# Kernel tuning notes

Hardware: AMD Instinct MI355X
Metric: run time of the kernel (lower is better)

Reference implementation:

```python
import jax, jax.numpy as jnp
import numpy as np

B, S = 64, 512
VOCAB, D, H, NH = 50000, 256, 256, 4
MAX_DUR = 12.0
SCALE_RATE = 1.0


def setup_inputs() -> dict:
    key = jax.random.key(0)
    ks = jax.random.split(key, 12)
    s = 1.0 / np.sqrt(H)
    inp = {
        "src": jax.random.randint(ks[0], (B, S), 0, VOCAB),
        "input_len": jax.random.randint(ks[1], (B,), 1, S + 1),
        "fix_src": jax.random.uniform(ks[2], (B, S), jnp.float32) * MAX_DUR,
        "emb_table": jax.random.normal(ks[3], (VOCAB, D), jnp.float32) * 0.02,
        "Wi": jax.random.uniform(ks[4], (H, D), jnp.float32, -s, s),
        "bi": jax.random.uniform(ks[5], (H,), jnp.float32, -s, s),
        "Wh": jax.random.uniform(ks[6], (H, NH * H), jnp.float32, -s, s),
        "bh": jax.random.uniform(ks[7], (H,), jnp.float32, -s, s),
        "fc1_W": jax.random.uniform(ks[8], (D, NH * H), jnp.float32, -s, s),
        "fc1_b": jax.random.uniform(ks[9], (D,), jnp.float32, -s, s),
        "fc2_W": jax.random.uniform(ks[10], (2, D), jnp.float32, -s, s),
        "fc2_b": jax.random.uniform(ks[11], (2,), jnp.float32, -s, s),
    }
    return inp


def _forward(src, input_len, fix_src, emb_table, Wi, bi, Wh, bh, fc1_W, fc1_b, fc2_W, fc2_b):
    emb = emb_table[src]                      # [B, S, D]
    offsets = jnp.arange(NH, dtype=emb.dtype) * (MAX_DUR / NH)  # [NH]
    h0 = jnp.zeros((NH, B, H), emb.dtype)

    def step(h, xd):
        x, d = xd                             # x [B,D], d [B]
        hcat = jnp.swapaxes(h, 0, 1).reshape(B, NH * H)
        cand = jnp.tanh(x @ Wi.T + bi + hcat @ Wh.T + bh)        # [B,H]
        g = jax.nn.sigmoid(d[:, None] * SCALE_RATE - offsets)    # [B,NH]
        gt = g.T[:, :, None]                                     # [NH,B,1]
        h_new = gt * cand[None, :, :] + (1.0 - gt) * h           # [NH,B,H]
        out = jnp.swapaxes(h_new, 0, 1).reshape(B, NH * H)
        return h_new, out

    xs = (jnp.swapaxes(emb, 0, 1), fix_src.T)  # [S,B,D], [S,B]
    _, outs = jax.lax.scan(step, h0, xs)       # [S, B, NH*H]
    outs = jnp.swapaxes(outs, 0, 1)            # [B, S, NH*H]
    sel = outs[jnp.arange(B), input_len - 1]   # gather at last valid step, [B, NH*H]
    hid = jnp.tanh(sel @ fc1_W.T + fc1_b)      # [B, D]
    return hid @ fc2_W.T + fc2_b               # [B, 2]


def reference(src, input_len, fix_src, emb_table, Wi, bi, Wh, bh, fc1_W, fc1_b, fc2_W, fc2_b):
    return _forward(src, input_len, fix_src, emb_table, Wi, bi, Wh, bh, fc1_W, fc1_b, fc2_W, fc2_b)
```

## Files before the change

kernel.cpp:

```cpp
#include <hip/hip_runtime.h>
#include <stdint.h>

constexpr int BB = 64;
constexpr int SS = 512;
constexpr int DD = 256;
constexpr int HH = 256;
constexpr int NHH = 4;
constexpr int KK = 1024;

constexpr int TT = 512;

typedef _Float16 f16;
typedef _Float16 f16x2 __attribute__((ext_vector_type(2)));
typedef _Float16 half8 __attribute__((ext_vector_type(8)));
typedef float f32x4 __attribute__((ext_vector_type(4)));

__device__ inline float dot2p(uint32_t a, uint32_t b, float c) {
  f16x2 av = __builtin_bit_cast(f16x2, a);
  f16x2 bv = __builtin_bit_cast(f16x2, b);
#if defined(__has_builtin)
#if __has_builtin(__builtin_amdgcn_fdot2)
  return __builtin_amdgcn_fdot2(av, bv, c, false);
#else
  return c + (float)av.x * (float)bv.x + (float)av.y * (float)bv.y;
#endif
#else
  return c + (float)av.x * (float)bv.x + (float)av.y * (float)bv.y;
#endif
}

__device__ inline float dot8(uint4 w, uint4 a, float c) {
  c = dot2p(w.x, a.x, c);
  c = dot2p(w.y, a.y, c);
  c = dot2p(w.z, a.z, c);
  c = dot2p(w.w, a.w, c);
  return c;
}

__device__ inline uint32_t pack2(float a, float b) {
  f16x2 v;
  v.x = (f16)a;
  v.y = (f16)b;
  return __builtin_bit_cast(uint32_t, v);
}

__device__ inline float fast_tanh(float x) {
  x = fminf(fmaxf(x, -15.f), 15.f);
  float e = __expf(2.f * x);
  return 1.f - 2.f / (e + 1.f);
}

__device__ __host__ inline int chunk_of(int p, int wv) {
  if (wv == 0) return 2 * p;
  if (wv == 7) return 2 * p + 1;
  return (2 * p + 1 + wv) & 7;
}

__global__ void k_pack_wq(const float* __restrict__ Wh, uint4* __restrict__ Wq) {
  int gid = blockIdx.x * blockDim.x + threadIdx.x;
  int p = gid >> 13;
  int m = (gid >> 9) & 15;
  int t = gid & 511;
  int j = m >> 2, u = m & 3;
  int wv = t >> 6, l = t & 63;
  int cw = chunk_of(p, wv);
  const float* s = Wh + (size_t)(64 * p + l) * KK + 256 * j + 32 * cw + 8 * u;
  uint4 w;
  w.x = pack2(s[0], s[1]);
  w.y = pack2(s[2], s[3]);
  w.z = pack2(s[4], s[5]);
  w.w = pack2(s[6], s[7]);
  Wq[gid] = w;
}

__global__ void k_transpose8(const float* __restrict__ src, float* __restrict__ dst,
                             int C, int total) {
  int gid = blockIdx.x * blockDim.x + threadIdx.x;
  if (gid >= total) return;
  int r = gid & 255, c = gid >> 8;
  dst[gid] = src[r * C + c];
}

__global__ void k_cvt_f16(const float* __restrict__ src, f16* __restrict__ dst,
                          int total) {
  int gid = blockIdx.x * blockDim.x + threadIdx.x;
  if (gid >= total) return;
  dst[gid] = (f16)src[gid];
}

__global__ __launch_bounds__(256) void k_u_mfma(
    const int* __restrict__ src, const float* __restrict__ emb,
    const f16* __restrict__ wif, const float* __restrict__ bi,
    const float* __restrict__ bh, const int* __restrict__ input_len,
    f16* __restrict__ U) {
  __shared__ __align__(16) char xls[32768];
  const int row0 = blockIdx.x * 64;
  const int b = row0 >> 9;
  if ((row0 & 511) >= input_len[b]) return;
  const int t = threadIdx.x;
  const int w = t >> 6, l = t & 63;

  for (int rr = 0; rr < 16; ++rr) {
    int r = w * 16 + rr;
    int srcid = src[row0 + r];
    const float4 x = *(const float4*)(emb + (size_t)srcid * DD + l * 4);
    uint2 dw;
    dw.x = pack2(x.x, x.y);
    dw.y = pack2(x.z, x.w);
    int byte = (r * 512 + l * 8) ^ ((r & 7) << 4);
    *(uint2*)(xls + byte) = dw;
  }
  __syncthreads();

  const int lm = l & 15, lk = l >> 4;
  const int arow = w * 16 + lm;
  const int xs = (arow & 7) << 4;

  for (int ct = 0; ct < 16; ++ct) {
    const int o = ct * 16 + lm;
    f32x4 acc = {0.f, 0.f, 0.f, 0.f};
    const f16* bp = wif + (size_t)o * 256 + lk * 8;
#pragma unroll
    for (int kt = 0; kt < 8; ++kt) {
      int ab = (arow * 512 + kt * 64 + lk * 16) ^ xs;
      half8 af = *(const half8*)(xls + ab);
      half8 bf = *(const half8*)(bp + kt * 32);
      acc = __builtin_amdgcn_mfma_f32_16x16x32_f16(af, bf, acc, 0, 0, 0);
    }
    float bias = bi[o] + bh[o];
#pragma unroll
    for (int reg = 0; reg < 4; ++reg) {
      int grow = row0 + w * 16 + lk * 4 + reg;
      U[(size_t)grow * HH + o] = (f16)(acc[reg] + bias);
    }
  }
}

__global__ void __attribute__((amdgpu_flat_work_group_size(512, 512),
                               amdgpu_waves_per_eu(2, 2)))
k_recurrence(
    const uint4* __restrict__ Wq, const f16* __restrict__ U,
    const float* __restrict__ fix_src, const int* __restrict__ input_len,
    const float* __restrict__ fc1T, const float* __restrict__ fc1_b,
    const float* __restrict__ fc2_W, const float* __restrict__ fc2_b,
    float* __restrict__ out, uint32_t* __restrict__ Cex,
    float* __restrict__ FPg, int* __restrict__ Flg) {
  __shared__ __align__(16) char arena[61440];
  f16* cbufX = (f16*)arena;
  uint4* cvecX = (uint4*)arena;
  float* part = (float*)(arena + 512);
  float* partials = (float*)(arena + 512);
  float* hbuf = (float*)(arena + 16896);
  float* fsbuf = (float*)(arena + 17920);

  const int idx = blockIdx.x;
  const int b = idx & 63;
  const int p = idx >> 6;
  const int t = threadIdx.x;
  const int wv = t >> 6, l = t & 63;
  const int out_i = t & 255, ch2 = t >> 8;

  const int cw = chunk_of(p, wv);
  const int q = cw >> 1, half = cw & 1;

  uint4 w[16];
  {
    const uint4* wp = Wq + (p * 16) * TT + t;
#pragma unroll
    for (int m = 0; m < 16; ++m) {
      const uint4* a = wp + m * TT;
      asm volatile("global_load_dwordx4 %0, %1, off"
                   : "=v"(w[m]) : "v"(a) : "memory");
    }
    asm volatile("s_waitcnt vmcnt(0)" ::: "memory");
  }

  float v0 = 0.f, v1 = 0.f, v2 = 0.f, v3 = 0.f;
  float h0 = 0.f, h1 = 0.f, h2 = 0.f, h3 = 0.f;
  float cprev = 0.f, unew = 0.f;

  const int len = input_len[b];
  const f16* Ub = U + (size_t)b * SS * HH;
  const float* fsb = fix_src + b * SS;

  fsbuf[t] = fsb[t];
  if (wv == 0) {
    float c0 = fast_tanh((float)Ub[64 * p + l]);
    f16 chv = (f16)c0;
    cprev = (float)chv;
    if (l < 32) cbufX[2 * p * 32 + l] = chv;
    uint32_t dwp =
        ((uint32_t)__builtin_bit_cast(unsigned short, chv) << 16) | 1u;
    __hip_atomic_store(&Cex[b * 256 + p * 64 + l], dwp, __ATOMIC_RELAXED,
                       __HIP_MEMORY_SCOPE_AGENT);
  }
  __syncthreads();

#pragma unroll 1
  for (int s = 0; s < len; ++s) {
#pragma unroll
    for (int m = 0; m < 16; ++m)
      asm volatile("" : "+v"(w[m].x), "+v"(w[m].y), "+v"(w[m].z), "+v"(w[m].w));

    const int par = s & 1;
    const uint32_t tag = (uint32_t)((s + 1) & 0xffff);
    float g0 = 0.f, g1 = 0.f, g2 = 0.f, g3 = 0.f;

    if (wv == 0) {
      const float dval = fsbuf[s];
      g0 = 1.f / (1.f + __expf(0.f - dval));
      g1 = 1.f / (1.f + __expf(3.f - dval));
      g2 = 1.f / (1.f + __expf(6.f - dval));
      g3 = 1.f / (1.f + __expf(9.f - dval));
      h0 = g0 * cprev + (1.f - g0) * h0;
      h1 = g1 * cprev + (1.f - g1) * h1;
      h2 = g2 * cprev + (1.f - g2) * h2;
      h3 = g3 * cprev + (1.f - g3) * h3;
      int sn = (s + 1 < len) ? (s + 1) : s;
      unew = (float)Ub[(size_t)sn * HH + 64 * p + l];
    } else {
      if (l < 32) {
        uint32_t* addr = &Cex[((par * 64 + b) * 4 + q) * 64 + 32 * half + l];
        uint32_t dw;
        do {
          dw = __hip_atomic_load(addr, __ATOMIC_RELAXED,
                                 __HIP_MEMORY_SCOPE_AGENT);
        } while ((dw & 0xffffu) != tag);
        cbufX[cw * 32 + l] = __builtin_bit_cast(f16, (unsigned short)(dw >> 16));
      }
    }

    {
      const uint4* ap = cvecX + cw * 4;
      uint4 a0 = ap[0], a1 = ap[1], a2 = ap[2], a3 = ap[3];
      float ac0 = 0.f, ac1 = 0.f, ac2 = 0.f, ac3 = 0.f;
      ac0 = dot8(w[0], a0, ac0);  ac0 = dot8(w[1], a1, ac0);
      ac0 = dot8(w[2], a2, ac0);  ac0 = dot8(w[3], a3, ac0);
      ac1 = dot8(w[4], a0, ac1);  ac1 = dot8(w[5], a1, ac1);
      ac1 = dot8(w[6], a2, ac1);  ac1 = dot8(w[7], a3, ac1);
      ac2 = dot8(w[8], a0, ac2);  ac2 = dot8(w[9], a1, ac2);
      ac2 = dot8(w[10], a2, ac2); ac2 = dot8(w[11], a3, ac2);
      ac3 = dot8(w[12], a0, ac3); ac3 = dot8(w[13], a1, ac3);
      ac3 = dot8(w[14], a2, ac3); ac3 = dot8(w[15], a3, ac3);
      float* pr = part + par * 2048 + cw * 256;
      pr[l] = ac0;
      pr[64 + l] = ac1;
      pr[128 + l] = ac2;
      pr[192 + l] = ac3;
    }
    __syncthreads();

    if (wv == 0) {
      float s0 = 0.f, s1 = 0.f, s2 = 0.f, s3 = 0.f;
      const float* pb = part + par * 2048;
#pragma unroll
      for (int kc = 0; kc < 8; ++kc) {
        const float* pr = pb + kc * 256;
        s0 += pr[l];
        s1 += pr[64 + l];
        s2 += pr[128 + l];
        s3 += pr[192 + l];
      }
      v0 = g0 * s0 + (1.f - g0) * v0;
      v1 = g1 * s1 + (1.f - g1) * v1;
      v2 = g2 * s2 + (1.f - g2) * v2;
      v3 = g3 * s3 + (1.f - g3) * v3;
      float c = fast_tanh(unew + (v0 + v1 + v2 + v3));
      f16 chv = (f16)c;
      cprev = (float)chv;
      uint32_t dwp =
          ((uint32_t)__builtin_bit_cast(unsigned short, chv) << 16) |
          (uint32_t)((s + 2) & 0xffff);
      __hip_atomic_store(&Cex[(((s + 1) & 1) * 64 + b) * 256 + p * 64 + l],
                         dwp, __ATOMIC_RELAXED, __HIP_MEMORY_SCOPE_AGENT);
      if (l < 32) cbufX[2 * p * 32 + l] = chv;
    }
  }

  if (wv == 0) {
    hbuf[l] = h0;
    hbuf[64 + l] = h1;
    hbuf[128 + l] = h2;
    hbuf[192 + l] = h3;
  }
  __syncthreads();
  {
    float acc = 0.f;
#pragma unroll 4
    for (int r = 0; r < 128; ++r) {
      int k_loc = ch2 * 128 + r;
      int n2 = k_loc >> 6, il = k_loc & 63;
      int kg = n2 * 256 + 64 * p + il;
      acc += hbuf[k_loc] * fc1T[(size_t)kg * 256 + out_i];
    }
    partials[t] = acc;
  }
  __syncthreads();
  if (t < 256) FPg[(b * 4 + p) * 256 + out_i] =
      partials[out_i] + partials[256 + out_i];
  __syncthreads();
  if (t == 0)
    __hip_atomic_store(&Flg[b * 4 + p], 0x5A5A5A5A, __ATOMIC_RELEASE,
                       __HIP_MEMORY_SCOPE_AGENT);
  if (p != 0) return;
  if (t < 4 && t > 0) {
    while (__hip_atomic_load(&Flg[b * 4 + t], __ATOMIC_ACQUIRE,
                             __HIP_MEMORY_SCOPE_AGENT) != 0x5A5A5A5A) {
    }
  }
  __syncthreads();
  if (t < 256) {
    float pre = fc1_b[t];
#pragma unroll
    for (int qq = 0; qq < 4; ++qq)
      pre += __hip_atomic_load(&FPg[(b * 4 + qq) * 256 + t], __ATOMIC_RELAXED,
                               __HIP_MEMORY_SCOPE_AGENT);
    hbuf[t] = fast_tanh(pre);
  }
  __syncthreads();
  if (t < 64) {
    float p0 = 0.f, p1 = 0.f;
    for (int oi = t; oi < 256; oi += 64) {
      float hh = hbuf[oi];
      p0 += hh * fc2_W[oi];
      p1 += hh * fc2_W[256 + oi];
    }
#pragma unroll
    for (int off = 32; off; off >>= 1) {
      p0 += __shfl_down(p0, off);
      p1 += __shfl_down(p1, off);
    }
    if (t == 0) {
      out[b * 2 + 0] = p0 + fc2_b[0];
      out[b * 2 + 1] = p1 + fc2_b[1];
    }
  }
}

extern "C" void kernel_launch(void* const* d_in, const int* in_sizes, int n_in,
                              void* d_out, int out_size, void* d_ws, size_t ws_size,
                              hipStream_t stream) {
  const int* src = (const int*)d_in[0];
  const int* input_len = (const int*)d_in[1];
  const float* fix_src = (const float*)d_in[2];
  const float* emb = (const float*)d_in[3];
  const float* Wi = (const float*)d_in[4];
  const float* bi = (const float*)d_in[5];
  const float* Wh = (const float*)d_in[6];
  const float* bh = (const float*)d_in[7];
  const float* fc1_W = (const float*)d_in[8];
  const float* fc1_b = (const float*)d_in[9];
  const float* fc2_W = (const float*)d_in[10];
  const float* fc2_b = (const float*)d_in[11];
  float* out = (float*)d_out;

  char* ws = (char*)d_ws;
  uint4* Wq = (uint4*)(ws);
  f16* wif = (f16*)(ws + (512ull << 10));
  float* fc1T = (float*)(ws + (768ull << 10));
  f16* U = (f16*)(ws + (1792ull << 10));
  uint32_t* Cex = (uint32_t*)(ws + (18176ull << 10));
  float* FPg = (float*)(ws + (18304ull << 10));
  int* Flg = (int*)(ws + (18560ull << 10));
  const size_t needed = (18561ull << 10);
  if (ws_size < needed) return;

  k_pack_wq<<<128, 256, 0, stream>>>(Wh, Wq);
  k_cvt_f16<<<(65536 + 255) / 256, 256, 0, stream>>>(Wi, wif, 65536);
  k_transpose8<<<(262144 + 255) / 256, 256, 0, stream>>>(fc1_W, fc1T, 1024, 262144);
  k_u_mfma<<<BB * SS / 64, 256, 0, stream>>>(src, emb, wif, bi, bh,
                                             input_len, U);
  k_recurrence<<<BB * 4, TT, 0, stream>>>(Wq, U, fix_src, input_len, fc1T,
                                          fc1_b, fc2_W, fc2_b, out, Cex, FPg,
                                          Flg);
}
```

Baseline: 704.7 us.

## Add L2-scoped fast path for cross-block exchange and co-locate batch blocks

```diff
diff --git a/kernel.cpp b/kernel.cpp
--- a/kernel.cpp
+++ b/kernel.cpp
@@ -48,6 +48,17 @@
   x = fminf(fmaxf(x, -15.f), 15.f);
   float e = __expf(2.f * x);
   return 1.f - 2.f / (e + 1.f);
+}
+
+__device__ inline uint32_t load_l2(const uint32_t* p) {
+  uint32_t v;
+  asm volatile("global_load_dword %0, %1, off sc0\n\ts_waitcnt vmcnt(0)"
+               : "=v"(v) : "v"(p) : "memory");
+  return v;
+}
+__device__ inline void store_l2(uint32_t* p, uint32_t v) {
+  asm volatile("global_store_dword %0, %1, off sc0"
+               :: "v"(p), "v"(v) : "memory");
 }
 
 __device__ __host__ inline int chunk_of(int p, int wv) {
@@ -144,7 +155,8 @@
     const float* __restrict__ fc1T, const float* __restrict__ fc1_b,
     const float* __restrict__ fc2_W, const float* __restrict__ fc2_b,
     float* __restrict__ out, uint32_t* __restrict__ Cex,
-    float* __restrict__ FPg, int* __restrict__ Flg) {
+    uint32_t* __restrict__ CexF, float* __restrict__ FPg,
+    int* __restrict__ Flg) {
   __shared__ __align__(16) char arena[61440];
   f16* cbufX = (f16*)arena;
   uint4* cvecX = (uint4*)arena;
@@ -154,8 +166,8 @@
   float* fsbuf = (float*)(arena + 17920);
 
   const int idx = blockIdx.x;
-  const int b = idx & 63;
-  const int p = idx >> 6;
+  const int b = idx >> 2;
+  const int p = idx & 3;
   const int t = threadIdx.x;
   const int wv = t >> 6, l = t & 63;
   const int out_i = t & 255, ch2 = t >> 8;
@@ -178,6 +190,8 @@
   float v0 = 0.f, v1 = 0.f, v2 = 0.f, v3 = 0.f;
   float h0 = 0.f, h1 = 0.f, h2 = 0.f, h3 = 0.f;
   float cprev = 0.f, unew = 0.f;
+  bool use_fast = true;
+  int fast_fail = 0;
 
   const int len = input_len[b];
   const f16* Ub = U + (size_t)b * SS * HH;
@@ -191,6 +205,7 @@
     if (l < 32) cbufX[2 * p * 32 + l] = chv;
     uint32_t dwp =
         ((uint32_t)__builtin_bit_cast(unsigned short, chv) << 16) | 1u;
+    store_l2(&CexF[b * 256 + p * 64 + l], dwp);
     __hip_atomic_store(&Cex[b * 256 + p * 64 + l], dwp, __ATOMIC_RELAXED,
                        __HIP_MEMORY_SCOPE_AGENT);
   }
@@ -220,12 +235,23 @@
       unew = (float)Ub[(size_t)sn * HH + 64 * p + l];
     } else {
       if (l < 32) {
-        uint32_t* addr = &Cex[((par * 64 + b) * 4 + q) * 64 + 32 * half + l];
-        uint32_t dw;
-        do {
-          dw = __hip_atomic_load(addr, __ATOMIC_RELAXED,
-                                 __HIP_MEMORY_SCOPE_AGENT);
-        } while ((dw & 0xffffu) != tag);
+        const int off = ((par * 64 + b) * 4 + q) * 64 + 32 * half + l;
+        uint32_t dw = 0;
+        bool got = false;
+        if (use_fast) {
+          int spins = (s < 4) ? 256 : 12;
+          do {
+            dw = load_l2(&CexF[off]);
+            got = ((dw & 0xffffu) == tag);
+          } while (!got && --spins);
+          if (!got && ++fast_fail >= 3) use_fast = false;
+        }
+        if (!got) {
+          do {
+            dw = __hip_atomic_load(&Cex[off], __ATOMIC_RELAXED,
+                                   __HIP_MEMORY_SCOPE_AGENT);
+          } while ((dw & 0xffffu) != tag);
+        }
         cbufX[cw * 32 + l] = __builtin_bit_cast(f16, (unsigned short)(dw >> 16));
       }
     }
@@ -271,8 +297,10 @@
       uint32_t dwp =
           ((uint32_t)__builtin_bit_cast(unsigned short, chv) << 16) |
           (uint32_t)((s + 2) & 0xffff);
-      __hip_atomic_store(&Cex[(((s + 1) & 1) * 64 + b) * 256 + p * 64 + l],
-                         dwp, __ATOMIC_RELAXED, __HIP_MEMORY_SCOPE_AGENT);
+      const int po = (((s + 1) & 1) * 64 + b) * 256 + p * 64 + l;
+      store_l2(&CexF[po], dwp);
+      __hip_atomic_store(&Cex[po], dwp, __ATOMIC_RELAXED,
+                         __HIP_MEMORY_SCOPE_AGENT);
       if (l < 32) cbufX[2 * p * 32 + l] = chv;
     }
   }
@@ -357,6 +385,7 @@
   char* ws = (char*)d_ws;
   uint4* Wq = (uint4*)(ws);
   f16* wif = (f16*)(ws + (512ull << 10));
+  uint32_t* CexF = (uint32_t*)(ws + (640ull << 10));
   float* fc1T = (float*)(ws + (768ull << 10));
   f16* U = (f16*)(ws + (1792ull << 10));
   uint32_t* Cex = (uint32_t*)(ws + (18176ull << 10));
@@ -371,6 +400,6 @@
   k_u_mfma<<<BB * SS / 64, 256, 0, stream>>>(src, emb, wif, bi, bh,
                                              input_len, U);
   k_recurrence<<<BB * 4, TT, 0, stream>>>(Wq, U, fix_src, input_len, fc1T,
-                                          fc1_b, fc2_W, fc2_b, out, Cex, FPg,
-                                          Flg);
-}
+                                          fc1_b, fc2_W, fc2_b, out, Cex, CexF,
+                                          FPg, Flg);
+}
```

New measurement: 868.4 us. +23.2%, slower.
